# Performance work log

Measured on AMD Instinct MI355X. Metric: run time of the kernel, lower is better.

## Reference

```python
import jax, jax.numpy as jnp
import numpy as np

MEM_DIM = 2048
MEM_FEAT = 512
N_TOKENS = 65536
ALPHA = 0.1
SOFTMAX_SCALE = 10.0


def _l2_normalize(x, axis, eps=1e-12):
    # matches tf.math.l2_normalize: x / sqrt(max(sum(x^2), eps))
    sq = jnp.sum(jnp.square(x), axis=axis, keepdims=True)
    return x * jax.lax.rsqrt(jnp.maximum(sq, eps))


def setup_inputs() -> dict:
    key = jax.random.key(0)
    k1, k2 = jax.random.split(key)
    inputs = jax.random.normal(k1, (N_TOKENS, MEM_FEAT), dtype=jnp.float32)
    memory = jax.random.normal(k2, (MEM_DIM, MEM_FEAT), dtype=jnp.float32) * 0.05
    return {"inputs": inputs, "memory": memory}


def reference(inputs, memory):
    inputs_norm = _l2_normalize(inputs, axis=1)            # [N, F]
    memory_norm = _l2_normalize(memory, axis=1)            # [M, F]
    cos_sim = jnp.einsum('nf,mf->nm', inputs_norm, memory_norm)  # [N, M]
    attn = jax.nn.softmax(cos_sim * SOFTMAX_SCALE, axis=1)       # [N, M]
    mem_update = jnp.einsum('nm,mf->nf', attn, memory_norm)      # [N, F]
    closest_idx = jnp.argmax(attn, axis=1)                       # [N]
    # one_hot^T @ inputs_norm == segment-sum of inputs_norm by closest code
    memory_updates = jax.ops.segment_sum(inputs_norm, closest_idx,
                                         num_segments=MEM_DIM)  # [M, F]
    updated_memory = memory * (1.0 - ALPHA) + memory_updates * ALPHA
    return mem_update, updated_memory
```

## Files before the change

kernel.cpp:

```cpp
#include <hip/hip_runtime.h>
#include <stdint.h>

#define N_TOK   65536
#define MDIM    2048
#define FDIM    512
#define SCALE_F 10.0f
#define TAU_BF  1.2e-3f
#define TAU_SP  2e-5f
#define QCAP    8192

typedef __attribute__((ext_vector_type(8))) unsigned short u16x8;
typedef __attribute__((ext_vector_type(4))) unsigned short u16x4;
typedef __attribute__((ext_vector_type(8))) __bf16 bf16x8;
typedef __attribute__((ext_vector_type(4))) float f32x4;

__device__ __forceinline__ unsigned short f2bf(float f) {
  unsigned int u = __builtin_bit_cast(unsigned int, f);
  u += 0x7fffu + ((u >> 16) & 1u);
  return (unsigned short)(u >> 16);
}
__device__ __forceinline__ float bf2f(unsigned short b) {
  return __builtin_bit_cast(float, (unsigned int)b << 16);
}
__device__ __forceinline__ f32x4 mfma16(u16x8 a, u16x8 b, f32x4 c) {
  return __builtin_amdgcn_mfma_f32_16x16x32_bf16(
      __builtin_bit_cast(bf16x8, a), __builtin_bit_cast(bf16x8, b), c, 0, 0, 0);
}
__device__ __forceinline__ void gload16(const unsigned short* g, unsigned short* l) {
  __builtin_amdgcn_global_load_lds(
      (const __attribute__((address_space(1))) unsigned int*)g,
      (__attribute__((address_space(3))) unsigned int*)l,
      16, 0, 0);
}
__device__ __forceinline__ unsigned long long packkey(float x, int col) {
  unsigned u = __builtin_bit_cast(unsigned, x);
  u = (u & 0x80000000u) ? ~u : (u | 0x80000000u);
  return ((unsigned long long)u << 32) | (unsigned)(2048 - col);
}
__device__ __forceinline__ float unpackval(unsigned long long k) {
  unsigned u = (unsigned)(k >> 32);
  u = (u & 0x80000000u) ? (u & 0x7fffffffu) : ~u;
  return __builtin_bit_cast(float, u);
}
__device__ __forceinline__ int unpackcol(unsigned long long k) {
  return 2048 - (int)(k & 0xffffffffu);
}
__device__ __forceinline__ void merge2(unsigned long long& k1, unsigned long long& k2,
                                       unsigned long long o1, unsigned long long o2) {
  if (o1 > k1) { k2 = (k1 > o2) ? k1 : o2; k1 = o1; }
  else if (o1 > k2) { k2 = o1; }
}
__device__ __forceinline__ int sslot(int colslot, int lrow) {
  return colslot ^ (lrow & 7);
}

__global__ __launch_bounds__(64) void zero_k(int* __restrict__ qcount) {
  if (threadIdx.x == 0) *qcount = 0;
}

__global__ __launch_bounds__(64) void prep_memory_k(
    const float* __restrict__ mem, unsigned short* __restrict__ Bh,
    unsigned short* __restrict__ Bl) {
  const int m = blockIdx.x;
  const int lane = threadIdx.x;
  const float* row = mem + (size_t)m * FDIM;
  float4 a = *(const float4*)(row + lane * 4);
  float4 b = *(const float4*)(row + 256 + lane * 4);
  float s = a.x * a.x + a.y * a.y + a.z * a.z + a.w * a.w +
            b.x * b.x + b.y * b.y + b.z * b.z + b.w * b.w;
  #pragma unroll
  for (int off = 1; off < 64; off <<= 1) s += __shfl_xor(s, off);
  const float rn = 1.0f / sqrtf(fmaxf(s, 1e-12f));
  float v[8] = {a.x, a.y, a.z, a.w, b.x, b.y, b.z, b.w};
  #pragma unroll
  for (int h = 0; h < 2; ++h) {
    ushort4 hs, lo;
    #pragma unroll
    for (int q = 0; q < 4; ++q) {
      float x = v[h * 4 + q] * rn;
      unsigned short hb = f2bf(x);
      ((unsigned short*)&hs)[q] = hb;
      ((unsigned short*)&lo)[q] = f2bf(x - bf2f(hb));
    }
    const size_t e = (size_t)m * FDIM + h * 256 + lane * 4;
    *(ushort4*)(Bh + e) = hs;
    *(ushort4*)(Bl + e) = lo;
  }
}

__global__ __launch_bounds__(256) void transpose_k(
    const unsigned short* __restrict__ Bh, unsigned short* __restrict__ Bt) {
  __shared__ unsigned short t[32][33];
  const int m0 = blockIdx.x * 32, f0 = blockIdx.y * 32;
  const int tx = threadIdx.x & 31, ty = threadIdx.x >> 5;
  #pragma unroll
  for (int r = ty; r < 32; r += 8)
    t[r][tx] = Bh[(size_t)(m0 + r) * FDIM + f0 + tx];
  __syncthreads();
  #pragma unroll
  for (int r = ty; r < 32; r += 8)
    Bt[(size_t)(f0 + r) * MDIM + m0 + tx] = t[tx][r];
}

__global__ __launch_bounds__(256) void prep_a_k(
    const float* __restrict__ inp, float* __restrict__ inv_n,
    unsigned short* __restrict__ Ah, int baseRow) {
  const int r = blockIdx.x * 4 + (threadIdx.x >> 6);
  const int lane = threadIdx.x & 63;
  const int grow = baseRow + r;
  const float* x = inp + (size_t)grow * FDIM;
  float4 a = *(const float4*)(x + lane * 4);
  float4 b = *(const float4*)(x + 256 + lane * 4);
  float s = a.x * a.x + a.y * a.y + a.z * a.z + a.w * a.w +
            b.x * b.x + b.y * b.y + b.z * b.z + b.w * b.w;
  #pragma unroll
  for (int off = 1; off < 64; off <<= 1) s += __shfl_xor(s, off);
  const float rn = 1.0f / sqrtf(fmaxf(s, 1e-12f));
  if (lane == 0) inv_n[grow] = rn;
  ushort4 h0, h1;
  h0.x = f2bf(a.x * rn); h0.y = f2bf(a.y * rn);
  h0.z = f2bf(a.z * rn); h0.w = f2bf(a.w * rn);
  h1.x = f2bf(b.x * rn); h1.y = f2bf(b.y * rn);
  h1.z = f2bf(b.z * rn); h1.w = f2bf(b.w * rn);
  *(ushort4*)(Ah + (size_t)r * FDIM + lane * 4) = h0;
  *(ushort4*)(Ah + (size_t)r * FDIM + 256 + lane * 4) = h1;
}

template <int MODE, bool SPLIT, bool SWZ>
__global__ __launch_bounds__(256) void gemm_bt_k(
    const unsigned short* __restrict__ Ah, const unsigned short* __restrict__ Al,
    const unsigned short* __restrict__ Bh, const unsigned short* __restrict__ Bl,
    void* __restrict__ Cv, int N, int K, int nbxLog2,
    const int* __restrict__ qlimit, float* __restrict__ ssum,
    unsigned long long* __restrict__ sk1, unsigned long long* __restrict__ sk2,
    const float* __restrict__ rowscale) {
  int wg = blockIdx.x;
  if (SWZ) {
    const int q = gridDim.x >> 3;
    wg = (wg & 7) * q + (wg >> 3);
  }
  const int bx = wg & ((1 << nbxLog2) - 1);
  const int by = wg >> nbxLog2;
  const int m0 = by * 128, n0 = bx * 128;
  if (qlimit) {
    int lim = *qlimit; if (lim > QCAP) lim = QCAP;
    lim = (lim + 127) & ~127;
    if (m0 >= lim) return;
  }
  constexpr int BUF_B = (SPLIT ? 4 : 2) * 8192;
  __shared__ alignas(16) char smem[2 * BUF_B];

  const int tid = threadIdx.x;
  const int lane = tid & 63, wave = tid >> 6;
  const int wr = wave >> 1, wc = wave & 1;
  const int lr = lane & 15, ls = lane >> 4;

  f32x4 acc[4][4] = {};

  const int row0 = wave * 32 + (lane >> 2);
  const int row1 = row0 + 16;
  const int ce = (lane & 3) * 8;
  const unsigned short* gA0 = Ah + (size_t)(m0 + row0) * K + ce;
  const unsigned short* gA1 = Ah + (size_t)(m0 + row1) * K + ce;
  const unsigned short* gB0 = Bh + (size_t)(n0 + row0) * K + ce;
  const unsigned short* gB1 = Bh + (size_t)(n0 + row1) * K + ce;
  const unsigned short* gAl0 = nullptr; const unsigned short* gAl1 = nullptr;
  const unsigned short* gBl0 = nullptr; const unsigned short* gBl1 = nullptr;
  if constexpr (SPLIT) {
    gAl0 = Al + (size_t)(m0 + row0) * K + ce;
    gAl1 = Al + (size_t)(m0 + row1) * K + ce;
    gBl0 = Bl + (size_t)(n0 + row0) * K + ce;
    gBl1 = Bl + (size_t)(n0 + row1) * K + ce;
  }

  auto stage = [&](int buf) {
    char* sb = smem + buf * BUF_B;
    unsigned short* bAh = (unsigned short*)sb;
    unsigned short* bBh = (unsigned short*)(sb + 8192);
    gload16(gA0, &bAh[wave * 1024]); gload16(gA1, &bAh[wave * 1024 + 512]);
    gload16(gB0, &bBh[wave * 1024]); gload16(gB1, &bBh[wave * 1024 + 512]);
    if constexpr (SPLIT) {
      unsigned short* bAl = (unsigned short*)(sb + 16384);
      unsigned short* bBl = (unsigned short*)(sb + 24576);
      gload16(gAl0, &bAl[wave * 1024]); gload16(gAl1, &bAl[wave * 1024 + 512]);
      gload16(gBl0, &bBl[wave * 1024]); gload16(gBl1, &bBl[wave * 1024 + 512]);
    }
    gA0 += 32; gA1 += 32; gB0 += 32; gB1 += 32;
    if constexpr (SPLIT) { gAl0 += 32; gAl1 += 32; gBl0 += 32; gBl1 += 32; }
  };

  const int nk = K >> 5;
  stage(0);
  __syncthreads();
  for (int ks = 0; ks < nk; ++ks) {
    const int cur = ks & 1;
    if (ks + 1 < nk) stage(cur ^ 1);
    const char* sb = smem + cur * BUF_B;
    const unsigned short* cAh = (const unsigned short*)sb;
    const unsigned short* cBh = (const unsigned short*)(sb + 8192);
    u16x8 fa[4], fb[4], fal[4], fbl[4];
    #pragma unroll
    for (int i = 0; i < 4; ++i) {
      const int ra = (wr * 64 + i * 16 + lr) * 32 + ls * 8;
      const int rb = (wc * 64 + i * 16 + lr) * 32 + ls * 8;
      fa[i] = *(const u16x8*)&cAh[ra];
      fb[i] = *(const u16x8*)&cBh[rb];
      if constexpr (SPLIT) {
        fal[i] = *(const u16x8*)&((const unsigned short*)(sb + 16384))[ra];
        fbl[i] = *(const u16x8*)&((const unsigned short*)(sb + 24576))[rb];
      }
    }
    #pragma unroll
    for (int i = 0; i < 4; ++i)
      #pragma unroll
      for (int j = 0; j < 4; ++j) {
        acc[i][j] = mfma16(fa[i], fb[j], acc[i][j]);
        if constexpr (SPLIT) {
          acc[i][j] = mfma16(fal[i], fb[j], acc[i][j]);
          acc[i][j] = mfma16(fa[i], fbl[j], acc[i][j]);
        }
      }
    __syncthreads();
  }

  if constexpr (MODE == 1) {
    unsigned short* P = (unsigned short*)Cv;
    float* sS = (float*)smem;
    #pragma unroll
    for (int ph = 0; ph < 4; ++ph) {
      __syncthreads();
      if (wr == (ph >> 1)) {
        const int ibase = (ph & 1) * 2;
        #pragma unroll
        for (int di = 0; di < 2; ++di)
          #pragma unroll
          for (int q = 0; q < 4; ++q) {
            const int lrow = di * 16 + ls * 4 + q;
            float* sr = &sS[lrow * 128];
            #pragma unroll
            for (int j = 0; j < 4; ++j) {
              const int col = wc * 64 + j * 16 + lr;
              sr[sslot(col >> 2, lrow) * 4 + (col & 3)] = acc[ibase + di][j][q];
            }
          }
      }
      __syncthreads();
      const int lrow = tid >> 3;
      const int h = tid & 7;
      const int grow = m0 + ph * 32 + lrow;
      const float* sr = &sS[lrow * 128];
      float esum = 0.f, m1v = -3.4e38f, m2v = -3.4e38f;
      int c1 = 2047;
      #pragma unroll
      for (int k = 0; k < 4; ++k) {
        const int lslot = k * 8 + h;
        const f32x4 v4 = *(const f32x4*)&sr[sslot(lslot, lrow) * 4];
        unsigned short pk4[4];
        #pragma unroll
        for (int e = 0; e < 4; ++e) {
          const float s = v4[e];
          const int col = n0 + lslot * 4 + e;
          if (s > m1v) { m2v = m1v; m1v = s; c1 = col; }
          else if (s > m2v) { m2v = s; }
          const float ex = __expf(SCALE_F * s);
          esum += ex;
          pk4[e] = f2bf(ex);
        }
        *(u16x4*)&P[(size_t)grow * N + n0 + lslot * 4] = *(u16x4*)pk4;
      }
      unsigned long long k1 = packkey(m1v, c1);
      unsigned long long k2 = packkey(m2v, 2047);
      #pragma unroll
      for (int off = 1; off < 8; off <<= 1) {
        const unsigned long long o1 = __shfl_xor(k1, off);
        const unsigned long long o2 = __shfl_xor(k2, off);
        esum += __shfl_xor(esum, off);
        merge2(k1, k2, o1, o2);
      }
      if (h == 0) {
        const size_t sp = (size_t)grow * 16 + bx;
        ssum[sp] = esum; sk1[sp] = k1; sk2[sp] = k2;
      }
    }
  } else {
    float* C = (float*)Cv;
    #pragma unroll
    for (int i = 0; i < 4; ++i) {
      const int rrow = m0 + wr * 64 + i * 16 + ls * 4;
      #pragma unroll
      for (int j = 0; j < 4; ++j) {
        const int col = n0 + wc * 64 + j * 16 + lr;
        #pragma unroll
        for (int q = 0; q < 4; ++q) {
          float v = acc[i][j][q];
          if constexpr (MODE == 2) v *= rowscale[rrow + q];
          C[(size_t)(rrow + q) * N + col] = v;
        }
      }
    }
  }
}

__global__ __launch_bounds__(256) void rowstat_k(
    const float* __restrict__ ssum, const unsigned long long* __restrict__ sk1,
    const unsigned long long* __restrict__ sk2, int* __restrict__ idx,
    float* __restrict__ rowinv, int* __restrict__ queue,
    int* __restrict__ qcount, int baseRow) {
  const int row = blockIdx.x * 16 + (threadIdx.x >> 4);
  const int p = threadIdx.x & 15;
  const size_t sp = (size_t)row * 16 + p;
  float sum = ssum[sp];
  unsigned long long k1 = sk1[sp], k2 = sk2[sp];
  #pragma unroll
  for (int off = 1; off < 16; off <<= 1) {
    const unsigned long long o1 = __shfl_xor(k1, off);
    const unsigned long long o2 = __shfl_xor(k2, off);
    sum += __shfl_xor(sum, off);
    merge2(k1, k2, o1, o2);
  }
  if (p == 0) {
    const int tok = baseRow + row;
    idx[tok] = unpackcol(k1);
    rowinv[row] = 1.0f / sum;
    if (unpackval(k1) - unpackval(k2) < TAU_BF) {
      int slot = atomicAdd(qcount, 1);
      if (slot < QCAP) queue[slot] = tok;
    }
  }
}

__global__ __launch_bounds__(256) void gather_prep_k(
    const int* __restrict__ queue, const int* __restrict__ qcount,
    const float* __restrict__ inp, const float* __restrict__ inv_n,
    unsigned short* __restrict__ Qh, unsigned short* __restrict__ Ql) {
  const int w = blockIdx.x * 4 + (threadIdx.x >> 6);
  const int lane = threadIdx.x & 63;
  int cnt = *qcount; if (cnt > QCAP) cnt = QCAP;
  if (w >= cnt) return;
  const int tok = queue[w];
  const float rn = inv_n[tok];
  const float* x = inp + (size_t)tok * FDIM;
  #pragma unroll
  for (int h = 0; h < 2; ++h) {
    float4 xv = *(const float4*)(x + h * 256 + lane * 4);
    float vv[4] = {xv.x, xv.y, xv.z, xv.w};
    ushort4 hs, lo;
    #pragma unroll
    for (int q = 0; q < 4; ++q) {
      float v = vv[q] * rn;
      unsigned short hb = f2bf(v);
      ((unsigned short*)&hs)[q] = hb;
      ((unsigned short*)&lo)[q] = f2bf(v - bf2f(hb));
    }
    const size_t e = (size_t)w * FDIM + h * 256 + lane * 4;
    *(ushort4*)(Qh + e) = hs;
    *(ushort4*)(Ql + e) = lo;
  }
}

__global__ __launch_bounds__(256) void refine2_k(
    const int* __restrict__ queue, const int* __restrict__ qcount,
    const float* __restrict__ Sref, const float* __restrict__ inp,
    const float* __restrict__ mem, int* __restrict__ idx) {
  const int w = blockIdx.x * 4 + (threadIdx.x >> 6);
  const int lane = threadIdx.x & 63;
  int cnt = *qcount; if (cnt > QCAP) cnt = QCAP;
  if (w >= cnt) return;
  const int tok = queue[w];
  const float* srow = Sref + (size_t)w * MDIM;
  float m1 = -3.4e38f, m2 = -3.4e38f;
  int i1 = 0x7fffffff, i2 = 0x7fffffff;
  #pragma unroll
  for (int i = 0; i < 8; ++i) {
    const float4 vv = *(const float4*)(srow + i * 256 + lane * 4);
    const float xs[4] = {vv.x, vv.y, vv.z, vv.w};
    #pragma unroll
    for (int q = 0; q < 4; ++q) {
      const float x = xs[q];
      const int ii = i * 256 + lane * 4 + q;
      if (x > m1 || (x == m1 && ii < i1)) { m2 = m1; i2 = i1; m1 = x; i1 = ii; }
      else if (x > m2 || (x == m2 && ii < i2)) { m2 = x; i2 = ii; }
    }
  }
  #pragma unroll
  for (int off = 1; off < 64; off <<= 1) {
    const float n1 = __shfl_xor(m1, off), n2 = __shfl_xor(m2, off);
    const int j1 = __shfl_xor(i1, off), j2 = __shfl_xor(i2, off);
    if (n1 > m1 || (n1 == m1 && j1 < i1)) {
      if (m1 > n2 || (m1 == n2 && i1 < j2)) { m2 = m1; i2 = i1; }
      else { m2 = n2; i2 = j2; }
      m1 = n1; i1 = j1;
    } else if (n1 > m2 || (n1 == m2 && j1 < i2)) { m2 = n1; i2 = j1; }
  }
  int pick = i1;
  if (m1 - m2 < TAU_SP) {
    const int a = (i1 < i2) ? i1 : i2, b = (i1 < i2) ? i2 : i1;
    const float* x = inp + (size_t)tok * FDIM;
    const float* ma = mem + (size_t)a * FDIM;
    const float* mb = mem + (size_t)b * FDIM;
    double da = 0, db = 0, na = 0, nb = 0;
    #pragma unroll
    for (int j = 0; j < 8; ++j) {
      const int e = lane * 8 + j;
      const double xv = x[e], av = ma[e], bv = mb[e];
      da += xv * av; na += av * av;
      db += xv * bv; nb += bv * bv;
    }
    #pragma unroll
    for (int off = 1; off < 64; off <<= 1) {
      da += __shfl_xor(da, off); na += __shfl_xor(na, off);
      db += __shfl_xor(db, off); nb += __shfl_xor(nb, off);
    }
    const double d1 = da / sqrt(fmax(na, 1e-12));
    const double d2 = db / sqrt(fmax(nb, 1e-12));
    if (d2 > d1) pick = b;
    else pick = a;
  }
  if (lane == 0) idx[tok] = pick;
}

__global__ __launch_bounds__(256) void segsum_k(
    const int* __restrict__ idx, const float* __restrict__ inp,
    const float* __restrict__ inv_n, float* __restrict__ updates) {
  __shared__ int lst[256];
  __shared__ int lcnt;
  const int m = blockIdx.x;
  const int t = threadIdx.x;
  float a0 = 0.f, a1 = 0.f;
  for (int base = 0; base < N_TOK; base += 4096) {
    if (t == 0) lcnt = 0;
    __syncthreads();
    #pragma unroll
    for (int u = 0; u < 4; ++u) {
      const int off4 = (u * 256 + t) * 4;
      const int4 v = *(const int4*)&idx[base + off4];
      if (v.x == m) { int p = atomicAdd(&lcnt, 1); if (p < 256) lst[p] = base + off4 + 0; }
      if (v.y == m) { int p = atomicAdd(&lcnt, 1); if (p < 256) lst[p] = base + off4 + 1; }
      if (v.z == m) { int p = atomicAdd(&lcnt, 1); if (p < 256) lst[p] = base + off4 + 2; }
      if (v.w == m) { int p = atomicAdd(&lcnt, 1); if (p < 256) lst[p] = base + off4 + 3; }
    }
    __syncthreads();
    int c = lcnt; if (c > 256) c = 256;
    if (t == 0 && c > 1) {
      for (int i = 1; i < c; ++i) {
        int key = lst[i], j = i - 1;
        while (j >= 0 && lst[j] > key) { lst[j + 1] = lst[j]; --j; }
        lst[j + 1] = key;
      }
    }
    __syncthreads();
    for (int i = 0; i < c; ++i) {
      const int tok = lst[i];
      const float rn = inv_n[tok];
      const float2 xv = *(const float2*)&inp[(size_t)tok * FDIM + t * 2];
      a0 += xv.x * rn; a1 += xv.y * rn;
    }
    __syncthreads();
  }
  *(float2*)&updates[(size_t)m * FDIM + t * 2] = make_float2(a0, a1);
}

__global__ __launch_bounds__(256) void final_update_k(
    const float* __restrict__ mem, const float* __restrict__ upd,
    float* __restrict__ out) {
  const size_t i = ((size_t)blockIdx.x * 256 + threadIdx.x) * 4;
  float4 m = *(const float4*)(mem + i);
  float4 u = *(const float4*)(upd + i);
  float4 r;
  r.x = m.x * 0.9f + u.x * 0.1f;
  r.y = m.y * 0.9f + u.y * 0.1f;
  r.z = m.z * 0.9f + u.z * 0.1f;
  r.w = m.w * 0.9f + u.w * 0.1f;
  *(float4*)(out + i) = r;
}

extern "C" void kernel_launch(void* const* d_in, const int* in_sizes, int n_in,
                              void* d_out, int out_size, void* d_ws, size_t ws_size,
                              hipStream_t stream) {
  const float* inputs = (const float*)d_in[0];
  const float* memory = (const float*)d_in[1];
  if (n_in >= 2 && in_sizes[0] != N_TOK * FDIM) {
    inputs = (const float*)d_in[1];
    memory = (const float*)d_in[0];
  }
  float* out_mu = (float*)d_out;
  float* out_um = out_mu + (size_t)N_TOK * FDIM;

  char* base = (char*)d_ws;
  size_t off = 0;
  auto take = [&](size_t bytes) -> char* {
    char* p = base + off;
    off = (off + bytes + 255) & ~(size_t)255;
    return p;
  };
  unsigned short* Bh = (unsigned short*)take((size_t)MDIM * FDIM * 2);
  unsigned short* Bl = (unsigned short*)take((size_t)MDIM * FDIM * 2);
  unsigned short* Bt = (unsigned short*)take((size_t)MDIM * FDIM * 2);
  float* inv_n = (float*)take((size_t)N_TOK * 4);
  float* updates = (float*)take((size_t)MDIM * FDIM * 4);
  int* idx = (int*)take((size_t)N_TOK * 4);
  int* queue = (int*)take((size_t)QCAP * 4);
  int* qcount = (int*)take(256);
  unsigned short* Qh = (unsigned short*)take((size_t)QCAP * FDIM * 2);
  unsigned short* Ql = (unsigned short*)take((size_t)QCAP * FDIM * 2);
  float* Sref = (float*)take((size_t)QCAP * MDIM * 4);
  const size_t fixed = off;

  int chunkT = 65536;
  while (chunkT > 128 && fixed + (size_t)chunkT * 5700 + 8192 > ws_size)
    chunkT >>= 1;
  if (fixed + (size_t)chunkT * 5700 + 8192 > ws_size) return;

  unsigned short* Ah = (unsigned short*)take((size_t)chunkT * FDIM * 2);
  unsigned short* Pbuf = (unsigned short*)take((size_t)chunkT * MDIM * 2);
  float* ssum = (float*)take((size_t)chunkT * 16 * 4);
  unsigned long long* sk1 = (unsigned long long*)take((size_t)chunkT * 16 * 8);
  unsigned long long* sk2 = (unsigned long long*)take((size_t)chunkT * 16 * 8);
  float* rowinv = (float*)take((size_t)chunkT * 4);

  zero_k<<<1, 64, 0, stream>>>(qcount);
  prep_memory_k<<<MDIM, 64, 0, stream>>>(memory, Bh, Bl);
  transpose_k<<<dim3(MDIM / 32, FDIM / 32), 256, 0, stream>>>(Bh, Bt);

  const int nby = chunkT / 128;
  for (int baseRow = 0; baseRow < N_TOK; baseRow += chunkT) {
    prep_a_k<<<chunkT / 4, 256, 0, stream>>>(inputs, inv_n, Ah, baseRow);
    gemm_bt_k<1, false, true><<<16 * nby, 256, 0, stream>>>(
        Ah, nullptr, Bh, nullptr, (void*)Pbuf, MDIM, FDIM, 4, nullptr,
        ssum, sk1, sk2, nullptr);
    rowstat_k<<<chunkT / 16, 256, 0, stream>>>(
        ssum, sk1, sk2, idx, rowinv, queue, qcount, baseRow);
    gemm_bt_k<2, false, true><<<4 * nby, 256, 0, stream>>>(
        Pbuf, nullptr, Bt, nullptr, (void*)(out_mu + (size_t)baseRow * FDIM),
        FDIM, MDIM, 2, nullptr, nullptr, nullptr, nullptr, rowinv);
  }
  gather_prep_k<<<QCAP / 4, 256, 0, stream>>>(queue, qcount, inputs, inv_n, Qh, Ql);
  gemm_bt_k<0, true, false><<<16 * (QCAP / 128), 256, 0, stream>>>(
      Qh, Ql, Bh, Bl, (void*)Sref, MDIM, FDIM, 4, qcount,
      nullptr, nullptr, nullptr, nullptr);
  refine2_k<<<QCAP / 4, 256, 0, stream>>>(queue, qcount, Sref, inputs, memory, idx);
  segsum_k<<<MDIM, 256, 0, stream>>>(idx, inputs, inv_n, updates);
  final_update_k<<<(MDIM * FDIM / 4) / 256, 256, 0, stream>>>(memory, updates, out_um);
}
```

Baseline: 751.1 us.

## Replace main GEMMs with 256x256-tile 8-wave pipelined kernel with swizzled LDS

Introduces gemm8p_k, a 512-thread GEMM with 256x256 output tiles, a BK=64 double-buffered LDS pipeline using XOR-swizzled layouts, explicit vmcnt waits, s_barrier phases and s_setprio around MFMA bursts. It is used for both the similarity/exp GEMM and the attention-times-memory GEMM. The per-row partial stats shrink from 16 to 8 column blocks, and rowstat_k is adjusted to match. The aim is more data reuse per tile and better overlap of global loads with MFMA work. In exchange it uses 128KB of LDS, which limits occupancy to one block per CU, and adds register pressure from a 32-accumulator tile.

```diff
diff --git a/kernel.cpp b/kernel.cpp
--- a/kernel.cpp
+++ b/kernel.cpp
@@ -49,9 +49,6 @@
                                        unsigned long long o1, unsigned long long o2) {
   if (o1 > k1) { k2 = (k1 > o2) ? k1 : o2; k1 = o1; }
   else if (o1 > k2) { k2 = o1; }
-}
-__device__ __forceinline__ int sslot(int colslot, int lrow) {
-  return colslot ^ (lrow & 7);
 }
 
 __global__ __launch_bounds__(64) void zero_k(int* __restrict__ qcount) {
@@ -126,28 +123,202 @@
   *(ushort4*)(Ah + (size_t)r * FDIM + 256 + lane * 4) = h1;
 }
 
-template <int MODE, bool SPLIT, bool SWZ>
-__global__ __launch_bounds__(256) void gemm_bt_k(
+template <int MODE>
+__global__ __launch_bounds__(512) void gemm8p_k(
+    const unsigned short* __restrict__ Am, const unsigned short* __restrict__ Bm,
+    void* __restrict__ Cv, int N, int K, int nbxLog2,
+    float* __restrict__ ssum, unsigned long long* __restrict__ sk1,
+    unsigned long long* __restrict__ sk2, const float* __restrict__ rowinv) {
+  __shared__ alignas(16) char smem[131072];
+  int wg = blockIdx.x;
+  { const int q = gridDim.x >> 3; wg = (wg & 7) * q + (wg >> 3); }
+  const int bx = wg & ((1 << nbxLog2) - 1);
+  const int by = wg >> nbxLog2;
+  const int m0 = by * 256, n0 = bx * 256;
+  const int tid = threadIdx.x;
+  const int lane = tid & 63, wid = tid >> 6;
+  const int wm = wid >> 2, wn = wid & 3;
+  const int lr = lane & 15, ls = lane >> 4;
+  const int c16 = (lane & 7) ^ (lane >> 3);
+  const int lrow8 = lane >> 3;
+
+  f32x4 acc[8][4] = {};
+  u16x8 bF[4][2];
+
+  const int NT = K >> 6;
+  const int niter = NT >> 1;
+
+  auto stageB = [&](int t, int half) {
+    char* dst0 = smem + (t & 1) * 65536 + 32768 + half * 16384;
+    #pragma unroll
+    for (int c = 0; c < 2; ++c) {
+      const int R = (wid * 2 + c) * 8;
+      const int rg = n0 + half * 128 + R + lrow8;
+      gload16(Bm + (size_t)rg * K + t * 64 + c16 * 8,
+              (unsigned short*)(dst0 + R * 128));
+    }
+  };
+  auto stageA = [&](int t, int q) {
+    const int half = wid >> 2;
+    const int R = q * 32 + (wid & 3) * 8;
+    char* dst = smem + (t & 1) * 65536 + half * 16384 + R * 128;
+    const int rg = m0 + half * 128 + R + lrow8;
+    gload16(Am + (size_t)rg * K + t * 64 + c16 * 8, (unsigned short*)dst);
+  };
+  auto ldsA = [&](int b, int rl, int ks) -> u16x8 {
+    const int p = (ks * 4 + ls) ^ (rl & 7);
+    return *(const u16x8*)(smem + b * 65536 + wm * 16384 + rl * 128 + p * 16);
+  };
+  auto ldsB = [&](int b, int rlb, int ks) -> u16x8 {
+    const int half = rlb >> 7, rl = rlb & 127;
+    const int p = (ks * 4 + ls) ^ (rl & 7);
+    return *(const u16x8*)(smem + b * 65536 + 32768 + half * 16384 + rl * 128 + p * 16);
+  };
+
+  stageB(0, 0); stageB(0, 1);
+  stageA(0, 0); stageA(0, 1); stageA(0, 2); stageA(0, 3);
+  stageB(1, 0); stageB(1, 1);
+  stageA(1, 0); stageA(1, 1); stageA(1, 2);
+
+  for (int it = 0; it < niter; ++it) {
+    const int T0 = 2 * it, T1 = T0 + 1;
+    #pragma unroll
+    for (int ph = 0; ph < 8; ++ph) {
+      const int tb = (ph < 4) ? 0 : 1;
+      const int ql = ph & 3;
+      if (ql == 0) {
+        if (ph == 4 && it == niter - 1)
+          asm volatile("s_waitcnt vmcnt(0)" ::: "memory");
+        else
+          asm volatile("s_waitcnt vmcnt(7)" ::: "memory");
+        __builtin_amdgcn_sched_barrier(0);
+        __builtin_amdgcn_s_barrier();
+        #pragma unroll
+        for (int nj = 0; nj < 4; ++nj)
+          #pragma unroll
+          for (int ks = 0; ks < 2; ++ks)
+            bF[nj][ks] = ldsB(tb, wn * 64 + nj * 16 + lr, ks);
+      } else {
+        __builtin_amdgcn_s_barrier();
+      }
+      u16x8 aF[2][2];
+      #pragma unroll
+      for (int di = 0; di < 2; ++di)
+        #pragma unroll
+        for (int ks = 0; ks < 2; ++ks)
+          aF[di][ks] = ldsA(tb, ql * 32 + di * 16 + lr, ks);
+      if (ph == 0) { if (T1 < NT) stageA(T1, 3); }
+      if (ph == 1) { if (T0 + 2 < NT) stageB(T0 + 2, 0); }
+      if (ph == 2) { if (T0 + 2 < NT) { stageB(T0 + 2, 1); stageA(T0 + 2, 0); } }
+      if (ph == 3) { if (T0 + 2 < NT) { stageA(T0 + 2, 1); stageA(T0 + 2, 2); } }
+      if (ph == 4) { if (T0 + 2 < NT) stageA(T0 + 2, 3); }
+      if (ph == 5) { if (T1 + 2 < NT) stageB(T1 + 2, 0); }
+      if (ph == 6) { if (T1 + 2 < NT) { stageB(T1 + 2, 1); stageA(T1 + 2, 0); } }
+      if (ph == 7) { if (T1 + 2 < NT) { stageA(T1 + 2, 1); stageA(T1 + 2, 2); } }
+      __builtin_amdgcn_s_setprio(1);
+      #pragma unroll
+      for (int di = 0; di < 2; ++di)
+        #pragma unroll
+        for (int nj = 0; nj < 4; ++nj)
+          #pragma unroll
+          for (int ks = 0; ks < 2; ++ks)
+            acc[ql * 2 + di][nj] = mfma16(aF[di][ks], bF[nj][ks], acc[ql * 2 + di][nj]);
+      __builtin_amdgcn_s_setprio(0);
+      __builtin_amdgcn_s_barrier();
+    }
+  }
+
+  if constexpr (MODE == 1) {
+    asm volatile("s_waitcnt vmcnt(0)" ::: "memory");
+    __builtin_amdgcn_sched_barrier(0);
+    __builtin_amdgcn_s_barrier();
+    unsigned short* P = (unsigned short*)Cv;
+    float* sc = (float*)smem;
+    #pragma unroll
+    for (int g = 0; g < 8; ++g) {
+      if ((wid >> 2) == (g >> 2)) {
+        const int di0 = (g & 3) * 2;
+        #pragma unroll
+        for (int di = 0; di < 2; ++di)
+          #pragma unroll
+          for (int nj = 0; nj < 4; ++nj)
+            #pragma unroll
+            for (int q = 0; q < 4; ++q)
+              sc[(di * 16 + ls * 4 + q) * 260 + wn * 64 + nj * 16 + lr] =
+                  acc[di0 + di][nj][q];
+      }
+      __syncthreads();
+      {
+        const int r = tid >> 4, cs = tid & 15;
+        const int grow = m0 + g * 32 + r;
+        float esum = 0.f, m1v = -3.4e38f, m2v = -3.4e38f;
+        int c1 = 0;
+        unsigned short pk[16];
+        #pragma unroll
+        for (int k = 0; k < 4; ++k) {
+          const f32x4 v = *(const f32x4*)&sc[r * 260 + cs * 16 + k * 4];
+          #pragma unroll
+          for (int e = 0; e < 4; ++e) {
+            const float s = v[e];
+            const int col = n0 + cs * 16 + k * 4 + e;
+            if (s > m1v) { m2v = m1v; m1v = s; c1 = col; }
+            else if (s > m2v) m2v = s;
+            const float ex = __expf(SCALE_F * s);
+            esum += ex;
+            pk[k * 4 + e] = f2bf(ex);
+          }
+        }
+        *(u16x8*)&P[(size_t)grow * N + n0 + cs * 16] = *(u16x8*)&pk[0];
+        *(u16x8*)&P[(size_t)grow * N + n0 + cs * 16 + 8] = *(u16x8*)&pk[8];
+        unsigned long long k1 = packkey(m1v, c1);
+        unsigned long long k2 = packkey(m2v, 2047);
+        #pragma unroll
+        for (int off = 1; off < 16; off <<= 1) {
+          const unsigned long long o1 = __shfl_xor(k1, off);
+          const unsigned long long o2 = __shfl_xor(k2, off);
+          esum += __shfl_xor(esum, off);
+          merge2(k1, k2, o1, o2);
+        }
+        if (cs == 0) {
+          const size_t sp = (size_t)grow * 8 + bx;
+          ssum[sp] = esum; sk1[sp] = k1; sk2[sp] = k2;
+        }
+      }
+      __syncthreads();
+    }
+  } else {
+    float* C = (float*)Cv;
+    #pragma unroll
+    for (int mi = 0; mi < 8; ++mi) {
+      const int rbase = m0 + wm * 128 + mi * 16 + ls * 4;
+      #pragma unroll
+      for (int q = 0; q < 4; ++q) {
+        const float ri = rowinv[rbase + q];
+        #pragma unroll
+        for (int nj = 0; nj < 4; ++nj) {
+          const int col = n0 + wn * 64 + nj * 16 + lr;
+          C[(size_t)(rbase + q) * N + col] = acc[mi][nj][q] * ri;
+        }
+      }
+    }
+  }
+}
+
+__global__ __launch_bounds__(256) void gemm_ref_k(
     const unsigned short* __restrict__ Ah, const unsigned short* __restrict__ Al,
     const unsigned short* __restrict__ Bh, const unsigned short* __restrict__ Bl,
-    void* __restrict__ Cv, int N, int K, int nbxLog2,
-    const int* __restrict__ qlimit, float* __restrict__ ssum,
-    unsigned long long* __restrict__ sk1, unsigned long long* __restrict__ sk2,
-    const float* __restrict__ rowscale) {
-  int wg = blockIdx.x;
-  if (SWZ) {
-    const int q = gridDim.x >> 3;
-    wg = (wg & 7) * q + (wg >> 3);
-  }
+    float* __restrict__ C, int N, int K, int nbxLog2,
+    const int* __restrict__ qlimit) {
+  const int wg = blockIdx.x;
   const int bx = wg & ((1 << nbxLog2) - 1);
   const int by = wg >> nbxLog2;
   const int m0 = by * 128, n0 = bx * 128;
-  if (qlimit) {
+  {
     int lim = *qlimit; if (lim > QCAP) lim = QCAP;
     lim = (lim + 127) & ~127;
     if (m0 >= lim) return;
   }
-  constexpr int BUF_B = (SPLIT ? 4 : 2) * 8192;
+  constexpr int BUF_B = 4 * 8192;
   __shared__ alignas(16) char smem[2 * BUF_B];
 
   const int tid = threadIdx.x;
@@ -164,29 +335,23 @@
   const unsigned short* gA1 = Ah + (size_t)(m0 + row1) * K + ce;
   const unsigned short* gB0 = Bh + (size_t)(n0 + row0) * K + ce;
   const unsigned short* gB1 = Bh + (size_t)(n0 + row1) * K + ce;
-  const unsigned short* gAl0 = nullptr; const unsigned short* gAl1 = nullptr;
-  const unsigned short* gBl0 = nullptr; const unsigned short* gBl1 = nullptr;
-  if constexpr (SPLIT) {
-    gAl0 = Al + (size_t)(m0 + row0) * K + ce;
-    gAl1 = Al + (size_t)(m0 + row1) * K + ce;
-    gBl0 = Bl + (size_t)(n0 + row0) * K + ce;
-    gBl1 = Bl + (size_t)(n0 + row1) * K + ce;
-  }
+  const unsigned short* gAl0 = Al + (size_t)(m0 + row0) * K + ce;
+  const unsigned short* gAl1 = Al + (size_t)(m0 + row1) * K + ce;
+  const unsigned short* gBl0 = Bl + (size_t)(n0 + row0) * K + ce;
+  const unsigned short* gBl1 = Bl + (size_t)(n0 + row1) * K + ce;
 
   auto stage = [&](int buf) {
     char* sb = smem + buf * BUF_B;
     unsigned short* bAh = (unsigned short*)sb;
     unsigned short* bBh = (unsigned short*)(sb + 8192);
+    unsigned short* bAl = (unsigned short*)(sb + 16384);
+    unsigned short* bBl = (unsigned short*)(sb + 24576);
     gload16(gA0, &bAh[wave * 1024]); gload16(gA1, &bAh[wave * 1024 + 512]);
     gload16(gB0, &bBh[wave * 1024]); gload16(gB1, &bBh[wave * 1024 + 512]);
-    if constexpr (SPLIT) {
-      unsigned short* bAl = (unsigned short*)(sb + 16384);
-      unsigned short* bBl = (unsigned short*)(sb + 24576);
-      gload16(gAl0, &bAl[wave * 1024]); gload16(gAl1, &bAl[wave * 1024 + 512]);
-      gload16(gBl0, &bBl[wave * 1024]); gload16(gBl1, &bBl[wave * 1024 + 512]);
-    }
+    gload16(gAl0, &bAl[wave * 1024]); gload16(gAl1, &bAl[wave * 1024 + 512]);
+    gload16(gBl0, &bBl[wave * 1024]); gload16(gBl1, &bBl[wave * 1024 + 512]);
     gA0 += 32; gA1 += 32; gB0 += 32; gB1 += 32;
-    if constexpr (SPLIT) { gAl0 += 32; gAl1 += 32; gBl0 += 32; gBl1 += 32; }
+    gAl0 += 32; gAl1 += 32; gBl0 += 32; gBl1 += 32;
   };
 
   const int nk = K >> 5;
@@ -196,107 +361,36 @@
     const int cur = ks & 1;
     if (ks + 1 < nk) stage(cur ^ 1);
     const char* sb = smem + cur * BUF_B;
-    const unsigned short* cAh = (const unsigned short*)sb;
-    const unsigned short* cBh = (const unsigned short*)(sb + 8192);
     u16x8 fa[4], fb[4], fal[4], fbl[4];
     #pragma unroll
     for (int i = 0; i < 4; ++i) {
       const int ra = (wr * 64 + i * 16 + lr) * 32 + ls * 8;
       const int rb = (wc * 64 + i * 16 + lr) * 32 + ls * 8;
-      fa[i] = *(const u16x8*)&cAh[ra];
-      fb[i] = *(const u16x8*)&cBh[rb];
-      if constexpr (SPLIT) {
-        fal[i] = *(const u16x8*)&((const unsigned short*)(sb + 16384))[ra];
-        fbl[i] = *(const u16x8*)&((const unsigned short*)(sb + 24576))[rb];
-      }
+      fa[i] = *(const u16x8*)&((const unsigned short*)sb)[ra];
+      fb[i] = *(const u16x8*)&((const unsigned short*)(sb + 8192))[rb];
+      fal[i] = *(const u16x8*)&((const unsigned short*)(sb + 16384))[ra];
+      fbl[i] = *(const u16x8*)&((const unsigned short*)(sb + 24576))[rb];
     }
     #pragma unroll
     for (int i = 0; i < 4; ++i)
       #pragma unroll
       for (int j = 0; j < 4; ++j) {
         acc[i][j] = mfma16(fa[i], fb[j], acc[i][j]);
-        if constexpr (SPLIT) {
-          acc[i][j] = mfma16(fal[i], fb[j], acc[i][j]);
-          acc[i][j] = mfma16(fa[i], fbl[j], acc[i][j]);
-        }
+        acc[i][j] = mfma16(fal[i], fb[j], acc[i][j]);
+        acc[i][j] = mfma16(fa[i], fbl[j], acc[i][j]);
       }
     __syncthreads();
   }
 
-  if constexpr (MODE == 1) {
-    unsigned short* P = (unsigned short*)Cv;
-    float* sS = (float*)smem;
-    #pragma unroll
-    for (int ph = 0; ph < 4; ++ph) {
-      __syncthreads();
-      if (wr == (ph >> 1)) {
-        const int ibase = (ph & 1) * 2;
-        #pragma unroll
-        for (int di = 0; di < 2; ++di)
-          #pragma unroll
-          for (int q = 0; q < 4; ++q) {
-            const int lrow = di * 16 + ls * 4 + q;
-            float* sr = &sS[lrow * 128];
-            #pragma unroll
-            for (int j = 0; j < 4; ++j) {
-              const int col = wc * 64 + j * 16 + lr;
-              sr[sslot(col >> 2, lrow) * 4 + (col & 3)] = acc[ibase + di][j][q];
-            }
-          }
-      }
-      __syncthreads();
-      const int lrow = tid >> 3;
-      const int h = tid & 7;
-      const int grow = m0 + ph * 32 + lrow;
-      const float* sr = &sS[lrow * 128];
-      float esum = 0.f, m1v = -3.4e38f, m2v = -3.4e38f;
-      int c1 = 2047;
+  #pragma unroll
+  for (int i = 0; i < 4; ++i) {
+    const int rrow = m0 + wr * 64 + i * 16 + ls * 4;
+    #pragma unroll
+    for (int j = 0; j < 4; ++j) {
+      const int col = n0 + wc * 64 + j * 16 + lr;
       #pragma unroll
-      for (int k = 0; k < 4; ++k) {
-        const int lslot = k * 8 + h;
-        const f32x4 v4 = *(const f32x4*)&sr[sslot(lslot, lrow) * 4];
-        unsigned short pk4[4];
-        #pragma unroll
-        for (int e = 0; e < 4; ++e) {
-          const float s = v4[e];
-          const int col = n0 + lslot * 4 + e;
-          if (s > m1v) { m2v = m1v; m1v = s; c1 = col; }
-          else if (s > m2v) { m2v = s; }
-          const float ex = __expf(SCALE_F * s);
-          esum += ex;
-          pk4[e] = f2bf(ex);
-        }
-        *(u16x4*)&P[(size_t)grow * N + n0 + lslot * 4] = *(u16x4*)pk4;
-      }
-      unsigned long long k1 = packkey(m1v, c1);
-      unsigned long long k2 = packkey(m2v, 2047);
-      #pragma unroll
-      for (int off = 1; off < 8; off <<= 1) {
-        const unsigned long long o1 = __shfl_xor(k1, off);
-        const unsigned long long o2 = __shfl_xor(k2, off);
-        esum += __shfl_xor(esum, off);
-        merge2(k1, k2, o1, o2);
-      }
-      if (h == 0) {
-        const size_t sp = (size_t)grow * 16 + bx;
-        ssum[sp] = esum; sk1[sp] = k1; sk2[sp] = k2;
-      }
-    }
-  } else {
-    float* C = (float*)Cv;
-    #pragma unroll
-    for (int i = 0; i < 4; ++i) {
-      const int rrow = m0 + wr * 64 + i * 16 + ls * 4;
-      #pragma unroll
-      for (int j = 0; j < 4; ++j) {
-        const int col = n0 + wc * 64 + j * 16 + lr;
-        #pragma unroll
-        for (int q = 0; q < 4; ++q) {
-          float v = acc[i][j][q];
-          if constexpr (MODE == 2) v *= rowscale[rrow + q];
-          C[(size_t)(rrow + q) * N + col] = v;
-        }
-      }
+      for (int q = 0; q < 4; ++q)
+        C[(size_t)(rrow + q) * N + col] = acc[i][j][q];
     }
   }
 }
@@ -306,13 +400,13 @@
     const unsigned long long* __restrict__ sk2, int* __restrict__ idx,
     float* __restrict__ rowinv, int* __restrict__ queue,
     int* __restrict__ qcount, int baseRow) {
-  const int row = blockIdx.x * 16 + (threadIdx.x >> 4);
-  const int p = threadIdx.x & 15;
-  const size_t sp = (size_t)row * 16 + p;
+  const int row = blockIdx.x * 32 + (threadIdx.x >> 3);
+  const int p = threadIdx.x & 7;
+  const size_t sp = (size_t)row * 8 + p;
   float sum = ssum[sp];
   unsigned long long k1 = sk1[sp], k2 = sk2[sp];
   #pragma unroll
-  for (int off = 1; off < 16; off <<= 1) {
+  for (int off = 1; off < 8; off <<= 1) {
     const unsigned long long o1 = __shfl_xor(k1, off);
     const unsigned long long o2 = __shfl_xor(k2, off);
     sum += __shfl_xor(sum, off);
@@ -507,37 +601,34 @@
   const size_t fixed = off;
 
   int chunkT = 65536;
-  while (chunkT > 128 && fixed + (size_t)chunkT * 5700 + 8192 > ws_size)
+  while (chunkT > 2048 && fixed + (size_t)chunkT * 5400 + 8192 > ws_size)
     chunkT >>= 1;
-  if (fixed + (size_t)chunkT * 5700 + 8192 > ws_size) return;
+  if (fixed + (size_t)chunkT * 5400 + 8192 > ws_size) return;
 
   unsigned short* Ah = (unsigned short*)take((size_t)chunkT * FDIM * 2);
   unsigned short* Pbuf = (unsigned short*)take((size_t)chunkT * MDIM * 2);
-  float* ssum = (float*)take((size_t)chunkT * 16 * 4);
-  unsigned long long* sk1 = (unsigned long long*)take((size_t)chunkT * 16 * 8);
-  unsigned long long* sk2 = (unsigned long long*)take((size_t)chunkT * 16 * 8);
+  float* ssum = (float*)take((size_t)chunkT * 8 * 4);
+  unsigned long long* sk1 = (unsigned long long*)take((size_t)chunkT * 8 * 8);
+  unsigned long long* sk2 = (unsigned long long*)take((size_t)chunkT * 8 * 8);
   float* rowinv = (float*)take((size_t)chunkT * 4);
 
   zero_k<<<1, 64, 0, stream>>>(qcount);
   prep_memory_k<<<MDIM, 64, 0, stream>>>(memory, Bh, Bl);
   transpose_k<<<dim3(MDIM / 32, FDIM / 32), 256, 0, stream>>>(Bh, Bt);
 
-  const int nby = chunkT / 128;
   for (int baseRow = 0; baseRow < N_TOK; baseRow += chunkT) {
     prep_a_k<<<chunkT / 4, 256, 0, stream>>>(inputs, inv_n, Ah, baseRow);
-    gemm_bt_k<1, false, true><<<16 * nby, 256, 0, stream>>>(
-        Ah, nullptr, Bh, nullptr, (void*)Pbuf, MDIM, FDIM, 4, nullptr,
-        ssum, sk1, sk2, nullptr);
-    rowstat_k<<<chunkT / 16, 256, 0, stream>>>(
+    gemm8p_k<1><<<(chunkT / 256) * 8, 512, 0, stream>>>(
+        Ah, Bh, (void*)Pbuf, MDIM, FDIM, 3, ssum, sk1, sk2, nullptr);
+    rowstat_k<<<chunkT / 32, 256, 0, stream>>>(
         ssum, sk1, sk2, idx, rowinv, queue, qcount, baseRow);
-    gemm_bt_k<2, false, true><<<4 * nby, 256, 0, stream>>>(
-        Pbuf, nullptr, Bt, nullptr, (void*)(out_mu + (size_t)baseRow * FDIM),
-        FDIM, MDIM, 2, nullptr, nullptr, nullptr, nullptr, rowinv);
+    gemm8p_k<2><<<(chunkT / 256) * 2, 512, 0, stream>>>(
+        Pbuf, Bt, (void*)(out_mu + (size_t)baseRow * FDIM), FDIM, MDIM, 1,
+        nullptr, nullptr, nullptr, rowinv);
   }
   gather_prep_k<<<QCAP / 4, 256, 0, stream>>>(queue, qcount, inputs, inv_n, Qh, Ql);
-  gemm_bt_k<0, true, false><<<16 * (QCAP / 128), 256, 0, stream>>>(
-      Qh, Ql, Bh, Bl, (void*)Sref, MDIM, FDIM, 4, qcount,
-      nullptr, nullptr, nullptr, nullptr);
+  gemm_ref_k<<<16 * (QCAP / 128), 256, 0, stream>>>(
+      Qh, Ql, Bh, Bl, Sref, MDIM, FDIM, 4, qcount);
   refine2_k<<<QCAP / 4, 256, 0, stream>>>(queue, qcount, Sref, inputs, memory, idx);
   segsum_k<<<MDIM, 256, 0, stream>>>(idx, inputs, inv_n, updates);
   final_update_k<<<(MDIM * FDIM / 4) / 256, 256, 0, stream>>>(memory, updates, out_um);
```

New measurement: 718.7 us. 4.3% less time.

## Replace P×M GEMM with 256x256-tile, 8-wave, finely pipelined kernel

Applied to the files above, without the earlier changes.

The second GEMM (attention probabilities times normalized memory) moves from the generic 128x128 templated kernel to a dedicated 512-thread kernel. It uses 256x256 output tiles, a 64-wide K step with double-buffered 128KB LDS, and staggered async global loads interleaved across eight phases, with explicit waitcnt, barriers and setprio around the MFMAs. The row-scale multiply moves into this new kernel's epilogue. The goal is more operand reuse per LDS load and better overlap of loads with MFMA, at the cost of high LDS and register use, which limits occupancy. The minimum chunk size is also raised to 2048 so the 256-row tiling always divides evenly.

```diff
diff --git a/kernel.cpp b/kernel.cpp
--- a/kernel.cpp
+++ b/kernel.cpp
@@ -132,8 +132,7 @@
     const unsigned short* __restrict__ Bh, const unsigned short* __restrict__ Bl,
     void* __restrict__ Cv, int N, int K, int nbxLog2,
     const int* __restrict__ qlimit, float* __restrict__ ssum,
-    unsigned long long* __restrict__ sk1, unsigned long long* __restrict__ sk2,
-    const float* __restrict__ rowscale) {
+    unsigned long long* __restrict__ sk1, unsigned long long* __restrict__ sk2) {
   int wg = blockIdx.x;
   if (SWZ) {
     const int q = gridDim.x >> 3;
@@ -291,11 +290,128 @@
       for (int j = 0; j < 4; ++j) {
         const int col = n0 + wc * 64 + j * 16 + lr;
         #pragma unroll
-        for (int q = 0; q < 4; ++q) {
-          float v = acc[i][j][q];
-          if constexpr (MODE == 2) v *= rowscale[rrow + q];
-          C[(size_t)(rrow + q) * N + col] = v;
-        }
+        for (int q = 0; q < 4; ++q)
+          C[(size_t)(rrow + q) * N + col] = acc[i][j][q];
+      }
+    }
+  }
+}
+
+__global__ __launch_bounds__(512) void gemm8p2_k(
+    const unsigned short* __restrict__ Am, const unsigned short* __restrict__ Bm,
+    float* __restrict__ C, int N, int K,
+    const float* __restrict__ rowinv) {
+  constexpr int NTT = 32;
+  constexpr int NITER = NTT / 2;
+  __shared__ alignas(16) char smem[131072];
+  int wg = blockIdx.x;
+  { const int q = gridDim.x >> 3; wg = (wg & 7) * q + (wg >> 3); }
+  const int bx0 = wg & 1;
+  const int by = wg >> 1;
+  const int m0 = by * 256;
+  const int tid = threadIdx.x;
+  const int lane = tid & 63, wid = tid >> 6;
+  const int wm = wid >> 2, wn = wid & 3;
+  const int lr = lane & 15, ls = lane >> 4;
+  const int c16 = (lane & 7) ^ (lane >> 3);
+  const int lrow8 = lane >> 3;
+
+  f32x4 acc[8][4] = {};
+  u16x8 bF[4][2];
+
+  auto stageB = [&](int T, int half) {
+    const int ko = T * 64;
+    char* dst0 = smem + (T & 1) * 65536 + 32768 + half * 16384;
+    #pragma unroll
+    for (int c = 0; c < 2; ++c) {
+      const int R = (wid * 2 + c) * 8;
+      const int rg = bx0 * 256 + half * 128 + R + lrow8;
+      gload16(Bm + (size_t)rg * K + ko + c16 * 8,
+              (unsigned short*)(dst0 + R * 128));
+    }
+  };
+  auto stageA = [&](int T, int q) {
+    const int ko = T * 64;
+    const int half = wid >> 2;
+    const int R = q * 32 + (wid & 3) * 8;
+    char* dst = smem + (T & 1) * 65536 + half * 16384 + R * 128;
+    const int rg = m0 + half * 128 + R + lrow8;
+    gload16(Am + (size_t)rg * K + ko + c16 * 8, (unsigned short*)dst);
+  };
+  auto ldsA = [&](int b, int rl, int ks) -> u16x8 {
+    const int p = (ks * 4 + ls) ^ (rl & 7);
+    return *(const u16x8*)(smem + b * 65536 + wm * 16384 + rl * 128 + p * 16);
+  };
+  auto ldsB = [&](int b, int rlb, int ks) -> u16x8 {
+    const int half = rlb >> 7, rl = rlb & 127;
+    const int p = (ks * 4 + ls) ^ (rl & 7);
+    return *(const u16x8*)(smem + b * 65536 + 32768 + half * 16384 + rl * 128 + p * 16);
+  };
+
+  stageB(0, 0); stageB(0, 1);
+  stageA(0, 0); stageA(0, 1); stageA(0, 2); stageA(0, 3);
+  stageB(1, 0); stageB(1, 1);
+  stageA(1, 0); stageA(1, 1); stageA(1, 2);
+
+  for (int it = 0; it < NITER; ++it) {
+    const int T0 = 2 * it, T1 = T0 + 1;
+    #pragma unroll
+    for (int ph = 0; ph < 8; ++ph) {
+      const int tb = (ph < 4) ? 0 : 1;
+      const int ql = ph & 3;
+      if (ql == 0) {
+        if (ph == 4 && it == NITER - 1)
+          asm volatile("s_waitcnt vmcnt(0)" ::: "memory");
+        else
+          asm volatile("s_waitcnt vmcnt(7)" ::: "memory");
+        __builtin_amdgcn_sched_barrier(0);
+        __builtin_amdgcn_s_barrier();
+        #pragma unroll
+        for (int nj = 0; nj < 4; ++nj)
+          #pragma unroll
+          for (int ks = 0; ks < 2; ++ks)
+            bF[nj][ks] = ldsB(tb, wn * 64 + nj * 16 + lr, ks);
+      } else {
+        __builtin_amdgcn_s_barrier();
+      }
+      u16x8 aF[2][2];
+      #pragma unroll
+      for (int di = 0; di < 2; ++di)
+        #pragma unroll
+        for (int ks = 0; ks < 2; ++ks)
+          aF[di][ks] = ldsA(tb, ql * 32 + di * 16 + lr, ks);
+      if (ph == 0) { if (T1 < NTT) stageA(T1, 3); }
+      if (ph == 1) { if (T0 + 2 < NTT) stageB(T0 + 2, 0); }
+      if (ph == 2) { if (T0 + 2 < NTT) { stageB(T0 + 2, 1); stageA(T0 + 2, 0); } }
+      if (ph == 3) { if (T0 + 2 < NTT) { stageA(T0 + 2, 1); stageA(T0 + 2, 2); } }
+      if (ph == 4) { if (T0 + 2 < NTT) stageA(T0 + 2, 3); }
+      if (ph == 5) { if (T1 + 2 < NTT) stageB(T1 + 2, 0); }
+      if (ph == 6) { if (T1 + 2 < NTT) { stageB(T1 + 2, 1); stageA(T1 + 2, 0); } }
+      if (ph == 7) { if (T1 + 2 < NTT) { stageA(T1 + 2, 1); stageA(T1 + 2, 2); } }
+      __builtin_amdgcn_s_setprio(1);
+      #pragma unroll
+      for (int di = 0; di < 2; ++di)
+        #pragma unroll
+        for (int nj = 0; nj < 4; ++nj)
+          #pragma unroll
+          for (int ks = 0; ks < 2; ++ks)
+            acc[ql * 2 + di][nj] = mfma16(aF[di][ks], bF[nj][ks], acc[ql * 2 + di][nj]);
+      __builtin_amdgcn_s_setprio(0);
+      __builtin_amdgcn_s_barrier();
+    }
+  }
+
+  const int n0 = bx0 * 256;
+  #pragma unroll
+  for (int mi = 0; mi < 8; ++mi) {
+    const int rbase = m0 + wm * 128 + mi * 16 + ls * 4;
+    #pragma unroll
+    for (int q = 0; q < 4; ++q) {
+      const float ri = rowinv[rbase + q];
+      #pragma unroll
+      for (int nj = 0; nj < 4; ++nj) {
+        const int col = n0 + wn * 64 + nj * 16 + lr;
+        C[(size_t)(rbase + q) * N + col] = acc[mi][nj][q] * ri;
       }
     }
   }
@@ -507,7 +623,7 @@
   const size_t fixed = off;
 
   int chunkT = 65536;
-  while (chunkT > 128 && fixed + (size_t)chunkT * 5700 + 8192 > ws_size)
+  while (chunkT > 2048 && fixed + (size_t)chunkT * 5700 + 8192 > ws_size)
     chunkT >>= 1;
   if (fixed + (size_t)chunkT * 5700 + 8192 > ws_size) return;
 
@@ -527,17 +643,16 @@
     prep_a_k<<<chunkT / 4, 256, 0, stream>>>(inputs, inv_n, Ah, baseRow);
     gemm_bt_k<1, false, true><<<16 * nby, 256, 0, stream>>>(
         Ah, nullptr, Bh, nullptr, (void*)Pbuf, MDIM, FDIM, 4, nullptr,
-        ssum, sk1, sk2, nullptr);
+        ssum, sk1, sk2);
     rowstat_k<<<chunkT / 16, 256, 0, stream>>>(
         ssum, sk1, sk2, idx, rowinv, queue, qcount, baseRow);
-    gemm_bt_k<2, false, true><<<4 * nby, 256, 0, stream>>>(
-        Pbuf, nullptr, Bt, nullptr, (void*)(out_mu + (size_t)baseRow * FDIM),
-        FDIM, MDIM, 2, nullptr, nullptr, nullptr, nullptr, rowinv);
+    gemm8p2_k<<<(chunkT / 256) * 2, 512, 0, stream>>>(
+        Pbuf, Bt, out_mu + (size_t)baseRow * FDIM, FDIM, MDIM, rowinv);
   }
   gather_prep_k<<<QCAP / 4, 256, 0, stream>>>(queue, qcount, inputs, inv_n, Qh, Ql);
   gemm_bt_k<0, true, false><<<16 * (QCAP / 128), 256, 0, stream>>>(
       Qh, Ql, Bh, Bl, (void*)Sref, MDIM, FDIM, 4, qcount,
-      nullptr, nullptr, nullptr, nullptr);
+      nullptr, nullptr, nullptr);
   refine2_k<<<QCAP / 4, 256, 0, stream>>>(queue, qcount, Sref, inputs, memory, idx);
   segsum_k<<<MDIM, 256, 0, stream>>>(idx, inputs, inv_n, updates);
   final_update_k<<<(MDIM * FDIM / 4) / 256, 256, 0, stream>>>(memory, updates, out_um);
```

New measurement: 726.3 us. 1.03x faster.
